# Performance work log

Measured on AMD Instinct MI355X. Metric: run time of the kernel, lower is better.

## Reference

```python
import jax, jax.numpy as jnp
import numpy as np
import itertools, math

M_MODES = 10
N_PHOT = 5
IN_MODES = np.array([0, 2, 4, 6, 8])  # input_state = [1,0,1,0,...], 5 photons
INV_SQRT2 = 0.7071067811865476

# Fock output bases (lexicographic ordering)
ROWS_NB = np.array(list(itertools.combinations(range(M_MODES), N_PHOT)), np.int32)          # [252,5] no-bunching
ROWS_B = np.array(list(itertools.combinations_with_replacement(range(M_MODES), N_PHOT)), np.int32)  # [2002,5] bunched

def _norms(rows):
    out = []
    for r in rows:
        c = np.bincount(r, minlength=M_MODES)
        out.append(float(np.prod([math.factorial(int(v)) for v in c])))
    return np.array(out, np.float32)

NORM_NB = _norms(ROWS_NB)  # all ones
NORM_B = _norms(ROWS_B)

# Glynn sign vectors for n=5 permanents (delta_0 fixed to +1): [16,5]
_D = np.array(list(itertools.product([1.0, -1.0], repeat=N_PHOT - 1)), np.float32)
DELTAS = np.concatenate([np.ones((_D.shape[0], 1), np.float32), _D], axis=1)
DSIGNS = np.prod(DELTAS, axis=1)


def _mzi(t1, t2):
    # BS // PS(t1) // BS // PS(t2); BS = (1/sqrt2)[[1,i],[i,1]], PS on first mode of pair
    B = jnp.array([[1.0, 1.0j], [1.0j, 1.0]], dtype=jnp.complex64) * INV_SQRT2
    e1 = jnp.exp(1j * t1)
    e2 = jnp.exp(1j * t2)
    M1 = B * jnp.stack([e1, jnp.ones_like(e1)])[:, None]   # PS(t1) @ BS
    M2 = B @ M1                                            # BS @ ...
    return M2 * jnp.stack([e2, jnp.ones_like(e2)])[:, None]  # PS(t2) @ ...


def interferometer(phases):
    """Rectangular (Clements) mesh on 10 modes with 45 MZIs; phases [45,2] -> U [10,10] complex."""
    Ts = jax.vmap(lambda p: _mzi(p[0], p[1]))(phases)  # [45,2,2]
    U = jnp.eye(M_MODES, dtype=jnp.complex64)
    k = 0
    for layer in range(M_MODES):
        for p in range(layer % 2, M_MODES - 1, 2):
            U = U.at[p:p + 2, :].set(Ts[k] @ U[p:p + 2, :])
            k += 1
    return U


def batched_permanent(Ms):
    """Glynn formula for [...,5,5] complex matrices."""
    D = jnp.asarray(DELTAS, dtype=Ms.dtype)       # [16,5]
    s = jnp.asarray(DSIGNS, dtype=Ms.dtype)       # [16]
    rowsum = jnp.einsum('di,...ij->...dj', D, Ms)  # [...,16,5]
    return jnp.einsum('d,...d->...', s, jnp.prod(rowsum, axis=-1)) / (2 ** (N_PHOT - 1))


def fock_probs(U, rows, norm):
    """U [B,10,10]; rows [K,5] output-mode indices (with repetition for bunching); norm [K]."""
    M = U[:, rows][..., IN_MODES]        # [B,K,5,5]
    perm = batched_permanent(M)          # [B,K]
    return (jnp.abs(perm) ** 2) / jnp.asarray(norm)


def _forward(x, W_down, b_down, phases_l1, phases_r1, phases_lf, phases_rf, W_out, b_out):
    h = (x @ W_down + b_down) / jnp.pi                 # downscale + DivideByPi -> [B,10]
    WL1 = interferometer(phases_l1)
    WR1 = interferometer(phases_r1)
    U1 = jnp.einsum('mk,bk,kn->bmn', WR1, jnp.exp(1j * h), WL1)  # WR @ diag(e^{i phi}) @ WL
    e1 = fock_probs(U1, ROWS_NB, NORM_NB)              # [B,252], no_bunching=True
    # final circuit: 252 px phase shifters round-robin over 10 modes -> phases add per mode
    Bsz = e1.shape[0]
    pad = jnp.pad(e1, ((0, 0), (0, 260 - 252)))
    phi2 = pad.reshape(Bsz, 26, M_MODES).sum(axis=1)   # [B,10]
    WLF = interferometer(phases_lf)
    WRF = interferometer(phases_rf)
    UF = jnp.einsum('mk,bk,kn->bmn', WRF, jnp.exp(1j * phi2), WLF)
    probs = fock_probs(UF, ROWS_B, NORM_B)             # [B,2002], bunched Fock states
    return probs @ W_out + b_out                       # [B,num_classes]


def setup_inputs() -> dict:
    key = jax.random.key(0)
    ks = jax.random.split(key, 9)
    two_pi = 2.0 * np.pi
    return {
        'x': jax.random.normal(ks[0], (128, 784), dtype=jnp.float32),
        'W_down': jax.random.normal(ks[1], (784, 10), dtype=jnp.float32) * 0.05,
        'b_down': jax.random.normal(ks[2], (10,), dtype=jnp.float32) * 0.05,
        'phases_l1': jax.random.uniform(ks[3], (45, 2), dtype=jnp.float32) * two_pi,
        'phases_r1': jax.random.uniform(ks[4], (45, 2), dtype=jnp.float32) * two_pi,
        'phases_lf': jax.random.uniform(ks[5], (45, 2), dtype=jnp.float32) * two_pi,
        'phases_rf': jax.random.uniform(ks[6], (45, 2), dtype=jnp.float32) * two_pi,
        'W_out': jax.random.normal(ks[7], (2002, 10), dtype=jnp.float32) * 0.02,
        'b_out': jax.random.normal(ks[8], (10,), dtype=jnp.float32) * 0.02,
    }


def reference(x, W_down, b_down, phases_l1, phases_r1, phases_lf, phases_rf, W_out, b_out):
    return _forward(x, W_down, b_down, phases_l1, phases_r1, phases_lf, phases_rf, W_out, b_out)
```

## Files before the change

### kernel.cpp

```cpp
#include <hip/hip_runtime.h>
#include <math.h>


#define PI_F 3.14159265358979323846f

__device__ __forceinline__ float2 cmul(float2 a, float2 b) {
  return make_float2(fmaf(a.x, b.x, -a.y * b.y), fmaf(a.x, b.y, a.y * b.x));
}
__device__ __forceinline__ float2 cadd(float2 a, float2 b) {
  return make_float2(a.x + b.x, a.y + b.y);
}
__device__ __forceinline__ float2 cscale(float2 a, float s) {
  return make_float2(a.x * s, a.y * s);
}
__device__ __forceinline__ float2 imul(float2 a) {
  return make_float2(-a.y, a.x);
}

__device__ __forceinline__ void unrank5f(int rank, float cnt0, float m0,
                                         int c[5]) {
  float r = (float)rank;
  float cnt = cnt0, m = m0, j = 4.f;
  int x = 0;
#pragma unroll
  for (int i = 0; i < 5; i++) {
    while (r >= cnt) {
      r -= cnt;
      cnt = cnt * (m - j) / m;
      m -= 1.f;
      x++;
    }
    c[i] = x;
    cnt = cnt * j / m;
    m -= 1.f;
    j -= 1.f;
    x++;
  }
}

__device__ __forceinline__ float2 prod5(const float2 rs[5]) {
  return cmul(cmul(cmul(rs[0], rs[1]), cmul(rs[2], rs[3])), rs[4]);
}

__device__ __forceinline__ float2 perm5(const float2 M[5][5]) {
  float2 rs[5];
#pragma unroll
  for (int j = 0; j < 5; j++) {
    rs[j] = M[0][j];
#pragma unroll
    for (int i = 1; i < 5; i++) rs[j] = cadd(rs[j], M[i][j]);
  }
  float2 acc = prod5(rs);
#pragma unroll
  for (int t = 1; t < 16; t++) {
    const int g = t ^ (t >> 1);
    const int bit = (t & 1) ? 0 : ((t & 2) ? 1 : ((t & 4) ? 2 : 3));
    const int i = bit + 1;
    const float step = ((g >> bit) & 1) ? -2.0f : 2.0f;
#pragma unroll
    for (int j = 0; j < 5; j++) {
      rs[j].x = fmaf(step, M[i][j].x, rs[j].x);
      rs[j].y = fmaf(step, M[i][j].y, rs[j].y);
    }
    float2 p = prod5(rs);
    const float s = (__popc(g) & 1) ? -1.0f : 1.0f;
    acc.x = fmaf(s, p.x, acc.x);
    acc.y = fmaf(s, p.y, acc.y);
  }
  return make_float2(acc.x * (1.0f / 16.0f), acc.y * (1.0f / 16.0f));
}

__global__ __launch_bounds__(256) void k_prefix(
    const float* __restrict__ x, const float* __restrict__ Wd,
    const float* __restrict__ bd, const float* __restrict__ ph_l1,
    const float* __restrict__ ph_r1, const float* __restrict__ ph_lf,
    const float* __restrict__ ph_rf, const float* __restrict__ bout,
    float2* __restrict__ UFws, float* __restrict__ out) {
  const int b = blockIdx.x, tid = threadIdx.x;

  __shared__ float2 T[4][45][4];
  __shared__ float2 Ui[4][100];
  __shared__ float2 Ub[100];
  __shared__ float  e1s[252];
  __shared__ float2 v[10];

  if (tid < 64) {
    if (tid < 40) {
      const int which = tid / 10, n = tid % 10;
      const float* ph = (which == 0) ? ph_l1
                      : (which == 1) ? ph_r1
                      : (which == 2) ? ph_lf : ph_rf;
#pragma unroll
      for (int t5 = 0; t5 < 5; t5++) {
        const int m = n + 10 * t5;
        if (m < 45) {
          float t1 = ph[m * 2 + 0], t2 = ph[m * 2 + 1];
          float s1, c1, s2, c2;
          __sincosf(t1, &s1, &c1);
          __sincosf(t2, &s2, &c2);
          float2 e2  = make_float2(c2, s2);
          float2 e1m = make_float2(c1 - 1.f, s1);
          float2 e1p = make_float2(c1 + 1.f, s1);
          T[which][m][0] = cscale(cmul(e2, e1m), 0.5f);
          T[which][m][1] = cscale(cmul(e2, imul(e1p)), 0.5f);
          T[which][m][2] = cscale(imul(e1p), 0.5f);
          T[which][m][3] = make_float2(0.5f * (1.f - c1), -0.5f * s1);
        }
      }
      float2 u[10];
#pragma unroll
      for (int m = 0; m < 10; m++)
        u[m] = make_float2(m == n ? 1.f : 0.f, 0.f);
      int kb = 0;
#pragma unroll
      for (int layer = 0; layer < 10; layer++) {
        const int start = layer & 1;
        const int npairs = 5 - start;
#pragma unroll
        for (int pi = 0; pi < 5; pi++) {
          if (pi < npairs) {
            const int p = start + 2 * pi;
            const int k = kb + pi;
            float2 u0 = u[p], u1 = u[p + 1];
            u[p]     = cadd(cmul(T[which][k][0], u0), cmul(T[which][k][1], u1));
            u[p + 1] = cadd(cmul(T[which][k][2], u0), cmul(T[which][k][3], u1));
          }
        }
        kb += npairs;
      }
#pragma unroll
      for (int m = 0; m < 10; m++) Ui[which][m * 10 + n] = u[m];
    }
  } else if (tid >= 128 && tid < 192) {
    const int lane = tid - 128;
    float acc[10];
#pragma unroll
    for (int c = 0; c < 10; c++) acc[c] = 0.f;
    const float4* x4 = (const float4*)(x + b * 784);
#pragma unroll
    for (int it = 0; it < 4; it++) {
      const int q = lane + it * 64;
      if (q < 196) {
        float4 xv = x4[q];
        const float4* w4 = (const float4*)(Wd + 40 * q);
        float W[40];
#pragma unroll
        for (int j = 0; j < 10; j++) {
          float4 wv = w4[j];
          W[4 * j + 0] = wv.x; W[4 * j + 1] = wv.y;
          W[4 * j + 2] = wv.z; W[4 * j + 3] = wv.w;
        }
        const float xe[4] = {xv.x, xv.y, xv.z, xv.w};
#pragma unroll
        for (int s = 0; s < 40; s++)
          acc[s % 10] = fmaf(xe[s / 10], W[s], acc[s % 10]);
      }
    }
#pragma unroll
    for (int d = 32; d > 0; d >>= 1)
#pragma unroll
      for (int c = 0; c < 10; c++) acc[c] += __shfl_xor(acc[c], d);
    if (lane < 10) {
      float s = (acc[lane] + bd[lane]) * (1.0f / PI_F);
      float sn, cs;
      __sincosf(s, &sn, &cs);
      v[lane] = make_float2(cs, sn);
    }
  }
  __syncthreads();

  if (tid < 100) {
    const int m = tid / 10, n = tid % 10;
    float2 acc = make_float2(0.f, 0.f);
#pragma unroll
    for (int k = 0; k < 10; k++)
      acc = cadd(acc, cmul(cmul(Ui[1][m * 10 + k], v[k]), Ui[0][k * 10 + n]));
    Ub[tid] = acc;
  }
  __syncthreads();

  if (tid < 252) {
    int c[5];
    unrank5f(tid, 126.f, 9.f, c);
    float2 M[5][5];
#pragma unroll
    for (int i = 0; i < 5; i++)
#pragma unroll
      for (int j = 0; j < 5; j++) M[i][j] = Ub[c[i] * 10 + 2 * j];
    float2 p = perm5(M);
    e1s[tid] = p.x * p.x + p.y * p.y;
  }
  __syncthreads();

  if (tid < 10) {
    float s = 0.f;
    for (int idx = tid; idx < 252; idx += 10) s += e1s[idx];
    float sn, cs;
    __sincosf(s, &sn, &cs);
    v[tid] = make_float2(cs, sn);
  }
  __syncthreads();

  if (tid < 100) {
    const int m = tid / 10, n = tid % 10;
    float2 acc = make_float2(0.f, 0.f);
#pragma unroll
    for (int k = 0; k < 10; k++)
      acc = cadd(acc, cmul(cmul(Ui[3][m * 10 + k], v[k]), Ui[2][k * 10 + n]));
    UFws[b * 100 + tid] = acc;
  }
  if (tid < 10) out[b * 10 + tid] = bout[tid];
}

__global__ __launch_bounds__(256) void k_perms(const float2* __restrict__ UFws,
                                               const float* __restrict__ Wout,
                                               float* __restrict__ out) {
  const int b = blockIdx.x >> 3, chunk = blockIdx.x & 7;
  const int tid = threadIdx.x;
  const int k = chunk * 256 + tid;
  __shared__ float2 U[100];
  __shared__ float red[4][10];
  if (tid < 50)
    ((float4*)U)[tid] = ((const float4*)(UFws + b * 100))[tid];
  __syncthreads();

  float acc[10];
#pragma unroll
  for (int c = 0; c < 10; c++) acc[c] = 0.f;

  if (k < 2002) {
    int c5[5];
    unrank5f(k, 715.f, 13.f, c5);
    int modes[5];
#pragma unroll
    for (int i = 0; i < 5; i++) modes[i] = c5[i] - i;
    float2 M[5][5];
#pragma unroll
    for (int i = 0; i < 5; i++)
#pragma unroll
      for (int j = 0; j < 5; j++) M[i][j] = U[modes[i] * 10 + 2 * j];
    float2 p = perm5(M);
    float norm = 1.f, cnt = 1.f;
#pragma unroll
    for (int i = 1; i < 5; i++) {
      cnt = (modes[i] == modes[i - 1]) ? cnt + 1.f : 1.f;
      norm *= cnt;
    }
    const float pv = (p.x * p.x + p.y * p.y) / norm;
    const float2* w2 = (const float2*)Wout + k * 5;
#pragma unroll
    for (int c = 0; c < 5; c++) {
      float2 w = w2[c];
      acc[2 * c + 0] = pv * w.x;
      acc[2 * c + 1] = pv * w.y;
    }
  }

  const int lane = tid & 63, wave = tid >> 6;
#pragma unroll
  for (int c = 0; c < 10; c++) {
    float r = acc[c];
#pragma unroll
    for (int d = 32; d > 0; d >>= 1) r += __shfl_down(r, d);
    if (lane == 0) red[wave][c] = r;
  }
  __syncthreads();
  if (tid < 10) {
    float s = red[0][tid] + red[1][tid] + red[2][tid] + red[3][tid];
    atomicAdd(&out[b * 10 + tid], s);
  }
}

extern "C" void kernel_launch(void* const* d_in, const int* in_sizes, int n_in,
                              void* d_out, int out_size, void* d_ws,
                              size_t ws_size, hipStream_t stream) {
  const float* x    = (const float*)d_in[0];
  const float* Wd   = (const float*)d_in[1];
  const float* bd   = (const float*)d_in[2];
  const float* pl1  = (const float*)d_in[3];
  const float* pr1  = (const float*)d_in[4];
  const float* plf  = (const float*)d_in[5];
  const float* prf  = (const float*)d_in[6];
  const float* Wout = (const float*)d_in[7];
  const float* bout = (const float*)d_in[8];
  float* out = (float*)d_out;

  float2* UFws = (float2*)d_ws;

  k_prefix<<<128, 256, 0, stream>>>(x, Wd, bd, pl1, pr1, plf, prf, bout, UFws,
                                    out);
  k_perms<<<1024, 256, 0, stream>>>(UFws, Wout, out);
}
```

Measured before the change: 86.11 us.

## Compute permanents via shared-memory Laplace-expansion DP and fuse both kernels

Replaces the per-output Glynn permanent evaluation with a level-by-level Laplace expansion DP over row subsets (and multisets for the bunched basis), stored in shared memory and sharing sub-permanents across outputs. The two launches are merged into one 512-thread block per sample, so the workspace round trip, the second launch and the atomics go away. The cost is only 128 blocks doing all 2002 outputs serially, plus several extra block barriers. The multiset normalisation changes from a divide to a multiply, which relies on the DP's repeated-row handling being consistent with it.

```diff
diff --git a/kernel.cpp b/kernel.cpp
--- a/kernel.cpp
+++ b/kernel.cpp
@@ -3,6 +3,7 @@
 
 
 #define PI_F 3.14159265358979323846f
+#define BLK 512
 
 __device__ __forceinline__ float2 cmul(float2 a, float2 b) {
   return make_float2(fmaf(a.x, b.x, -a.y * b.y), fmaf(a.x, b.y, a.y * b.x));
@@ -17,13 +18,14 @@
   return make_float2(-a.y, a.x);
 }
 
-__device__ __forceinline__ void unrank5f(int rank, float cnt0, float m0,
-                                         int c[5]) {
+template <int K>
+__device__ __forceinline__ void unrankT(int rank, float cnt0, float m0,
+                                        int c[5]) {
   float r = (float)rank;
-  float cnt = cnt0, m = m0, j = 4.f;
+  float cnt = cnt0, m = m0, j = (float)(K - 1);
   int x = 0;
 #pragma unroll
-  for (int i = 0; i < 5; i++) {
+  for (int i = 0; i < K; i++) {
     while (r >= cnt) {
       r -= cnt;
       cnt = cnt * (m - j) / m;
@@ -38,51 +40,77 @@
   }
 }
 
-__device__ __forceinline__ float2 prod5(const float2 rs[5]) {
-  return cmul(cmul(cmul(rs[0], rs[1]), cmul(rs[2], rs[3])), rs[4]);
-}
-
-__device__ __forceinline__ float2 perm5(const float2 M[5][5]) {
-  float2 rs[5];
-#pragma unroll
-  for (int j = 0; j < 5; j++) {
-    rs[j] = M[0][j];
-#pragma unroll
-    for (int i = 1; i < 5; i++) rs[j] = cadd(rs[j], M[i][j]);
-  }
-  float2 acc = prod5(rs);
-#pragma unroll
-  for (int t = 1; t < 16; t++) {
-    const int g = t ^ (t >> 1);
-    const int bit = (t & 1) ? 0 : ((t & 2) ? 1 : ((t & 4) ? 2 : 3));
-    const int i = bit + 1;
-    const float step = ((g >> bit) & 1) ? -2.0f : 2.0f;
-#pragma unroll
-    for (int j = 0; j < 5; j++) {
-      rs[j].x = fmaf(step, M[i][j].x, rs[j].x);
-      rs[j].y = fmaf(step, M[i][j].y, rs[j].y);
-    }
-    float2 p = prod5(rs);
-    const float s = (__popc(g) & 1) ? -1.0f : 1.0f;
-    acc.x = fmaf(s, p.x, acc.x);
-    acc.y = fmaf(s, p.y, acc.y);
-  }
-  return make_float2(acc.x * (1.0f / 16.0f), acc.y * (1.0f / 16.0f));
-}
-
-__global__ __launch_bounds__(256) void k_prefix(
+template <int K, bool MULTI>
+__device__ __forceinline__ float2 dp_gather(const int c[5],
+                                            const float2* __restrict__ prev,
+                                            const float2* __restrict__ Ublk,
+                                            const int* __restrict__ BL) {
+  const int col = 2 * (K - 1);
+  const int base = BL[(MULTI ? (8 + K) : 10) * 6 + (K - 1)] - 1;
+  int sufa[6];
+  sufa[K - 1] = 0;
+#pragma unroll
+  for (int j = K - 1; j >= 1; j--)
+    sufa[j - 1] = sufa[j] + BL[((MULTI ? (8 + K) : 9) - c[j]) * 6 + (K - j)];
+  float2 acc = make_float2(0.f, 0.f);
+  int pa = 0;
+#pragma unroll
+  for (int p = 0; p < K; p++) {
+    const int mp = MULTI ? (c[p] - p) : c[p];
+    bool take = true;
+    if (MULTI && p > 0) take = ((c[p] - p) != (c[p - 1] - (p - 1)));
+    if (take) {
+      const int R = base - pa - sufa[p];
+      acc = cadd(acc, cmul(prev[R], Ublk[mp * 10 + col]));
+    }
+    if (p < K - 1)
+      pa += BL[((MULTI ? (7 + K) : 9) - c[p]) * 6 + (K - 1 - p)];
+  }
+  return acc;
+}
+
+template <int K, bool MULTI>
+__device__ __forceinline__ void dp_level(int tid, int size, float cnt0,
+                                         float m0,
+                                         const float2* __restrict__ prev,
+                                         float2* __restrict__ cur,
+                                         const float2* __restrict__ Ublk,
+                                         const int* __restrict__ BL) {
+  for (int r = tid; r < size; r += BLK) {
+    int c[5];
+    unrankT<K>(r, cnt0, m0, c);
+    cur[r] = dp_gather<K, MULTI>(c, prev, Ublk, BL);
+  }
+}
+
+__global__ __launch_bounds__(BLK) void k_fused(
     const float* __restrict__ x, const float* __restrict__ Wd,
     const float* __restrict__ bd, const float* __restrict__ ph_l1,
     const float* __restrict__ ph_r1, const float* __restrict__ ph_lf,
     const float* __restrict__ ph_rf, const float* __restrict__ bout,
-    float2* __restrict__ UFws, float* __restrict__ out) {
+    const float* __restrict__ Wout, float* __restrict__ out) {
   const int b = blockIdx.x, tid = threadIdx.x;
 
   __shared__ float2 T[4][45][4];
   __shared__ float2 Ui[4][100];
   __shared__ float2 Ub[100];
+  __shared__ float2 dpA[220];
+  __shared__ float2 dpB[715];
   __shared__ float  e1s[252];
   __shared__ float2 v[10];
+  __shared__ float  red[BLK / 64][10];
+  __shared__ int    BL[14 * 6];
+
+  if (tid < 14) {
+    const int a = tid;
+    int val = 1;
+    BL[a * 6 + 0] = 1;
+#pragma unroll
+    for (int bb = 1; bb < 6; bb++) {
+      val = (a >= bb) ? val * (a - bb + 1) / bb : 0;
+      BL[a * 6 + bb] = val;
+    }
+  }
 
   if (tid < 64) {
     if (tid < 40) {
@@ -179,16 +207,19 @@
   }
   __syncthreads();
 
-  if (tid < 252) {
+  if (tid < 10) dpA[tid] = Ub[tid * 10];
+  __syncthreads();
+  dp_level<2, false>(tid, 45, 9.f, 9.f, dpA, dpB, Ub, BL);
+  __syncthreads();
+  dp_level<3, false>(tid, 120, 36.f, 9.f, dpB, dpA, Ub, BL);
+  __syncthreads();
+  dp_level<4, false>(tid, 210, 84.f, 9.f, dpA, dpB, Ub, BL);
+  __syncthreads();
+  for (int r = tid; r < 252; r += BLK) {
     int c[5];
-    unrank5f(tid, 126.f, 9.f, c);
-    float2 M[5][5];
-#pragma unroll
-    for (int i = 0; i < 5; i++)
-#pragma unroll
-      for (int j = 0; j < 5; j++) M[i][j] = Ub[c[i] * 10 + 2 * j];
-    float2 p = perm5(M);
-    e1s[tid] = p.x * p.x + p.y * p.y;
+    unrankT<5>(r, 126.f, 9.f, c);
+    float2 a = dp_gather<5, false>(c, dpB, Ub, BL);
+    e1s[r] = a.x * a.x + a.y * a.y;
   }
   __syncthreads();
 
@@ -207,67 +238,56 @@
 #pragma unroll
     for (int k = 0; k < 10; k++)
       acc = cadd(acc, cmul(cmul(Ui[3][m * 10 + k], v[k]), Ui[2][k * 10 + n]));
-    UFws[b * 100 + tid] = acc;
-  }
-  if (tid < 10) out[b * 10 + tid] = bout[tid];
-}
-
-__global__ __launch_bounds__(256) void k_perms(const float2* __restrict__ UFws,
-                                               const float* __restrict__ Wout,
-                                               float* __restrict__ out) {
-  const int b = blockIdx.x >> 3, chunk = blockIdx.x & 7;
-  const int tid = threadIdx.x;
-  const int k = chunk * 256 + tid;
-  __shared__ float2 U[100];
-  __shared__ float red[4][10];
-  if (tid < 50)
-    ((float4*)U)[tid] = ((const float4*)(UFws + b * 100))[tid];
-  __syncthreads();
-
-  float acc[10];
-#pragma unroll
-  for (int c = 0; c < 10; c++) acc[c] = 0.f;
-
-  if (k < 2002) {
+    Ub[tid] = acc;
+  }
+  __syncthreads();
+
+  if (tid < 10) dpA[tid] = Ub[tid * 10];
+  __syncthreads();
+  dp_level<2, true>(tid, 55, 10.f, 10.f, dpA, dpB, Ub, BL);
+  __syncthreads();
+  dp_level<3, true>(tid, 220, 55.f, 11.f, dpB, dpA, Ub, BL);
+  __syncthreads();
+  dp_level<4, true>(tid, 715, 220.f, 12.f, dpA, dpB, Ub, BL);
+  __syncthreads();
+
+  float accO[10];
+#pragma unroll
+  for (int c = 0; c < 10; c++) accO[c] = 0.f;
+  for (int r = tid; r < 2002; r += BLK) {
     int c5[5];
-    unrank5f(k, 715.f, 13.f, c5);
-    int modes[5];
-#pragma unroll
-    for (int i = 0; i < 5; i++) modes[i] = c5[i] - i;
-    float2 M[5][5];
-#pragma unroll
-    for (int i = 0; i < 5; i++)
-#pragma unroll
-      for (int j = 0; j < 5; j++) M[i][j] = U[modes[i] * 10 + 2 * j];
-    float2 p = perm5(M);
+    unrankT<5>(r, 715.f, 13.f, c5);
+    float2 a = dp_gather<5, true>(c5, dpB, Ub, BL);
     float norm = 1.f, cnt = 1.f;
 #pragma unroll
     for (int i = 1; i < 5; i++) {
-      cnt = (modes[i] == modes[i - 1]) ? cnt + 1.f : 1.f;
+      cnt = ((c5[i] - i) == (c5[i - 1] - (i - 1))) ? cnt + 1.f : 1.f;
       norm *= cnt;
     }
-    const float pv = (p.x * p.x + p.y * p.y) / norm;
-    const float2* w2 = (const float2*)Wout + k * 5;
-#pragma unroll
-    for (int c = 0; c < 5; c++) {
-      float2 w = w2[c];
-      acc[2 * c + 0] = pv * w.x;
-      acc[2 * c + 1] = pv * w.y;
-    }
-  }
-
-  const int lane = tid & 63, wave = tid >> 6;
+    const float pv = (a.x * a.x + a.y * a.y) * norm;
+    const float2* w2 = (const float2*)Wout + r * 5;
+#pragma unroll
+    for (int j = 0; j < 5; j++) {
+      float2 w = w2[j];
+      accO[2 * j + 0] = fmaf(pv, w.x, accO[2 * j + 0]);
+      accO[2 * j + 1] = fmaf(pv, w.y, accO[2 * j + 1]);
+    }
+  }
+
+  const int lane = tid & 63, wv = tid >> 6;
 #pragma unroll
   for (int c = 0; c < 10; c++) {
-    float r = acc[c];
-#pragma unroll
-    for (int d = 32; d > 0; d >>= 1) r += __shfl_down(r, d);
-    if (lane == 0) red[wave][c] = r;
+    float rsum = accO[c];
+#pragma unroll
+    for (int d = 32; d > 0; d >>= 1) rsum += __shfl_down(rsum, d);
+    if (lane == 0) red[wv][c] = rsum;
   }
   __syncthreads();
   if (tid < 10) {
-    float s = red[0][tid] + red[1][tid] + red[2][tid] + red[3][tid];
-    atomicAdd(&out[b * 10 + tid], s);
+    float s = bout[tid];
+#pragma unroll
+    for (int w = 0; w < BLK / 64; w++) s += red[w][tid];
+    out[b * 10 + tid] = s;
   }
 }
 
@@ -285,9 +305,7 @@
   const float* bout = (const float*)d_in[8];
   float* out = (float*)d_out;
 
-  float2* UFws = (float2*)d_ws;
-
-  k_prefix<<<128, 256, 0, stream>>>(x, Wd, bd, pl1, pr1, plf, prf, bout, UFws,
-                                    out);
-  k_perms<<<1024, 256, 0, stream>>>(UFws, Wout, out);
-}
+  (void)d_ws; (void)ws_size;
+  k_fused<<<128, BLK, 0, stream>>>(x, Wd, bd, pl1, pr1, plf, prf, bout, Wout,
+                                   out);
+}
```

Measured after the change: 95.95 us. 1.11x slower.
